# Kernel optimization log

Hardware: AMD Instinct MI355X
Metric: run time of the kernel (lower is better)

Reference implementation:

```python
import jax, jax.numpy as jnp
import numpy as np

B, L, E = 256, 500, 300  # bsz, max_doc_len, word_embed_dim
KS = [3, 5, 7]           # filters_size


def setup_inputs() -> dict:
    key = jax.random.key(0)
    ks = jax.random.split(key, 1 + 2 * len(KS))
    inp = {"x": jax.random.normal(ks[0], (B, L, E), jnp.float32)}
    i = 1
    for k in KS:
        # PyTorch Conv2d default init scale ~ 1/sqrt(fan_in)
        inp[f"aw{k}"] = jax.random.normal(ks[i], (k, E), jnp.float32) / np.sqrt(k * E).astype(np.float32); i += 1
        inp[f"ab{k}"] = jnp.zeros((1,), jnp.float32)
        inp[f"cw{k}"] = jax.random.normal(ks[i], (E,), jnp.float32) / np.sqrt(E).astype(np.float32); i += 1
        inp[f"cb{k}"] = jnpp = jnp.zeros((1,), jnp.float32)
    return inp


def _branch(x, aw, ab, cw, cb):
    # x: (B, L, E); aw: (k, E); cw: (E,)
    k = aw.shape[0]
    p = (k - 1) // 2
    x4 = x[:, None, :, :]            # NCHW: (B, 1, L, E)
    w4 = aw[None, None, :, :]        # OIHW: (1, 1, k, E)
    s = jax.lax.conv_general_dilated(x4, w4, window_strides=(1, 1),
                                     padding=((p, p), (0, 0)))  # (B, 1, L, 1)
    score = jax.nn.sigmoid(s + ab[0])[:, 0, :, :]               # (B, L, 1)
    gated = x * score                                           # broadcast over E
    # Conv2d(1,1,(1,E)) == per-timestep dot product over E
    return jnp.tanh(jnp.einsum('ble,e->bl', gated, cw) + cb[0])  # (B, L)


def reference(x, aw3, ab3, cw3, cb3, aw5, ab5, cw5, cb5, aw7, ab7, cw7, cb7):
    return (_branch(x, aw3, ab3, cw3, cb3),
            _branch(x, aw5, ab5, cw5, cb5),
            _branch(x, aw7, ab7, cw7, cb7))
```

## Files before the change

### kernel.cpp

```cpp
#include <hip/hip_runtime.h>
#include <math.h>

#define BB 256
#define LL 500
#define EE 300
#define NROWS (BB * LL)
#define ND 18
#define WSTR 20
#define KT 16
#define NTILES 19
#define KPAD (NTILES * KT)
#define WR 64
#define OPW 58
#define JPB 9
#define XSTR 17
#define DSTR 19


__global__ void wt_transpose(
    const float* __restrict__ aw3, const float* __restrict__ aw5,
    const float* __restrict__ aw7, const float* __restrict__ cw3,
    const float* __restrict__ cw5, const float* __restrict__ cw7,
    float* __restrict__ wt)
{
    const int idx = blockIdx.x * 256 + threadIdx.x;
    if (idx >= KPAD * WSTR) return;
    const int k = idx / WSTR;
    const int d = idx - k * WSTR;
    float v = 0.0f;
    if (k < EE && d < ND) {
        if      (d < 3)  v = aw3[d * EE + k];
        else if (d == 3) v = cw3[k];
        else if (d < 9)  v = aw5[(d - 4) * EE + k];
        else if (d == 9) v = cw5[k];
        else if (d < 17) v = aw7[(d - 10) * EE + k];
        else             v = cw7[k];
    }
    wt[idx] = v;
}

__global__ __launch_bounds__(256) void fused_kernel(
    const float* __restrict__ x, const float* __restrict__ wt,
    const float* __restrict__ ab3, const float* __restrict__ cb3,
    const float* __restrict__ ab5, const float* __restrict__ cb5,
    const float* __restrict__ ab7, const float* __restrict__ cb7,
    float* __restrict__ out)
{
    __shared__ float xlds[4][2][WR * XSTR];

    const int tid   = threadIdx.x;
    const int wave  = tid >> 6;
    const int lane  = tid & 63;
    const int job   = blockIdx.x * 4 + wave;
    const int batch = job / JPB;
    const int t     = job - batch * JPB;
    const int l0    = t * OPW - 3;

    const float* xbb = x + (size_t)batch * LL * EE;
    float* xw = &xlds[wave][0][0];

    const int srow = lane >> 2;
    const int sc   = lane & 3;

    const float* srp[4];
#pragma unroll
    for (int p = 0; p < 4; ++p) {
        int l = l0 + srow + p * 16;
        l = l < 0 ? 0 : (l >= LL ? LL - 1 : l);
        srp[p] = xbb + (size_t)l * EE;
    }

    float4 g[4];
#pragma unroll
    for (int p = 0; p < 4; ++p) g[p] = *(const float4*)(srp[p] + sc * 4);
#pragma unroll
    for (int p = 0; p < 4; ++p) {
        const int base = (srow + p * 16) * XSTR + sc * 4;
        xw[base + 0] = g[p].x; xw[base + 1] = g[p].y;
        xw[base + 2] = g[p].z; xw[base + 3] = g[p].w;
    }

    float acc[ND];
#pragma unroll
    for (int d = 0; d < ND; ++d) acc[d] = 0.0f;

#pragma unroll 1
    for (int tt = 0; tt < NTILES; ++tt) {
        const int nt = tt + 1;
        if (nt < NTILES) {
            const int k0 = nt * KT;
            const bool tail = (nt == NTILES - 1) && (sc == 3);
#pragma unroll
            for (int p = 0; p < 4; ++p) {
                if (tail) { g[p].x = 0.f; g[p].y = 0.f; g[p].z = 0.f; g[p].w = 0.f; }
                else      { g[p] = *(const float4*)(srp[p] + k0 + sc * 4); }
            }
        }

        const float* xb   = xw + (tt & 1) * (WR * XSTR) + lane * XSTR;
        const float* wrow = wt + tt * KT * WSTR;

        float xv[KT];
#pragma unroll
        for (int kk = 0; kk < KT; ++kk) xv[kk] = xb[kk];
#pragma unroll
        for (int kk = 0; kk < KT; ++kk) {
#pragma unroll
            for (int d = 0; d < ND; ++d)
                acc[d] = fmaf(wrow[kk * WSTR + d], xv[kk], acc[d]);
        }

        if (nt < NTILES) {
            float* xn = xw + (nt & 1) * (WR * XSTR);
#pragma unroll
            for (int p = 0; p < 4; ++p) {
                const int base = (srow + p * 16) * XSTR + sc * 4;
                xn[base + 0] = g[p].x; xn[base + 1] = g[p].y;
                xn[base + 2] = g[p].z; xn[base + 3] = g[p].w;
            }
        }
    }

    {
        const int lg = l0 + lane;
        const float vf = (lg >= 0 && lg < LL) ? 1.0f : 0.0f;
#pragma unroll
        for (int d = 0; d < ND; ++d) xw[lane * DSTR + d] = acc[d] * vf;
    }
    asm volatile("s_waitcnt lgkmcnt(0)" ::: "memory");

    if (lane >= 3 && lane < 3 + OPW) {
        const int lo = l0 + lane;
        if (lo < LL) {
            const int r = batch * LL + lo;
            const float cen3 = xw[lane * DSTR + 3];
            const float cen5 = xw[lane * DSTR + 9];
            const float cen7 = xw[lane * DSTR + 17];
            {
                float pre = 0.0f;
#pragma unroll
                for (int tp = 0; tp < 3; ++tp) pre += xw[(lane + tp - 1) * DSTR + tp];
                const float s = 1.0f / (1.0f + expf(-(pre + ab3[0])));
                out[r] = tanhf(s * cen3 + cb3[0]);
            }
            {
                float pre = 0.0f;
#pragma unroll
                for (int tp = 0; tp < 5; ++tp) pre += xw[(lane + tp - 2) * DSTR + 4 + tp];
                const float s = 1.0f / (1.0f + expf(-(pre + ab5[0])));
                out[NROWS + r] = tanhf(s * cen5 + cb5[0]);
            }
            {
                float pre = 0.0f;
#pragma unroll
                for (int tp = 0; tp < 7; ++tp) pre += xw[(lane + tp - 3) * DSTR + 10 + tp];
                const float s = 1.0f / (1.0f + expf(-(pre + ab7[0])));
                out[2 * NROWS + r] = tanhf(s * cen7 + cb7[0]);
            }
        }
    }
}

extern "C" void kernel_launch(void* const* d_in, const int* in_sizes, int n_in,
                              void* d_out, int out_size, void* d_ws, size_t ws_size,
                              hipStream_t stream) {
    const float* x   = (const float*)d_in[0];
    const float* aw3 = (const float*)d_in[1];
    const float* ab3 = (const float*)d_in[2];
    const float* cw3 = (const float*)d_in[3];
    const float* cb3 = (const float*)d_in[4];
    const float* aw5 = (const float*)d_in[5];
    const float* ab5 = (const float*)d_in[6];
    const float* cw5 = (const float*)d_in[7];
    const float* cb5 = (const float*)d_in[8];
    const float* aw7 = (const float*)d_in[9];
    const float* ab7 = (const float*)d_in[10];
    const float* cw7 = (const float*)d_in[11];
    const float* cb7 = (const float*)d_in[12];

    float* wt  = (float*)d_ws;
    float* out = (float*)d_out;

    wt_transpose<<<(KPAD * WSTR + 255) / 256, 256, 0, stream>>>(
        aw3, aw5, aw7, cw3, cw5, cw7, wt);

    fused_kernel<<<(BB * JPB) / 4, 256, 0, stream>>>(
        x, wt, ab3, cb3, ab5, cb5, ab7, cb7, out);
}
```

Before: 292.2 us.

## Split output channels across waves sharing one block-wide LDS x tile

```diff
diff --git a/kernel.cpp b/kernel.cpp
--- a/kernel.cpp
+++ b/kernel.cpp
@@ -5,16 +5,16 @@
 #define LL 500
 #define EE 300
 #define NROWS (BB * LL)
-#define ND 18
-#define WSTR 20
-#define KT 16
-#define NTILES 19
-#define KPAD (NTILES * KT)
+#define NDP 20
+#define NDW 5
+#define KT 32
+#define NT 10
+#define KPAD (NT * KT)
 #define WR 64
 #define OPW 58
 #define JPB 9
-#define XSTR 17
-#define DSTR 19
+#define XSTR 33
+#define DSTR 21
 
 
 __global__ void wt_transpose(
@@ -24,11 +24,11 @@
     float* __restrict__ wt)
 {
     const int idx = blockIdx.x * 256 + threadIdx.x;
-    if (idx >= KPAD * WSTR) return;
-    const int k = idx / WSTR;
-    const int d = idx - k * WSTR;
+    if (idx >= NDP * KPAD) return;
+    const int d = idx / KPAD;
+    const int k = idx - d * KPAD;
     float v = 0.0f;
-    if (k < EE && d < ND) {
+    if (k < EE && d < 18) {
         if      (d < 3)  v = aw3[d * EE + k];
         else if (d == 3) v = cw3[k];
         else if (d < 9)  v = aw5[(d - 4) * EE + k];
@@ -46,114 +46,105 @@
     const float* __restrict__ ab7, const float* __restrict__ cb7,
     float* __restrict__ out)
 {
-    __shared__ float xlds[4][2][WR * XSTR];
+    __shared__ float xlds[2][WR * XSTR];
+    __shared__ float dlds[WR * DSTR];
 
     const int tid   = threadIdx.x;
     const int wave  = tid >> 6;
     const int lane  = tid & 63;
-    const int job   = blockIdx.x * 4 + wave;
-    const int batch = job / JPB;
-    const int t     = job - batch * JPB;
+    const int batch = blockIdx.x / JPB;
+    const int t     = blockIdx.x - batch * JPB;
     const int l0    = t * OPW - 3;
 
     const float* xbb = x + (size_t)batch * LL * EE;
-    float* xw = &xlds[wave][0][0];
 
-    const int srow = lane >> 2;
-    const int sc   = lane & 3;
-
-    const float* srp[4];
-#pragma unroll
-    for (int p = 0; p < 4; ++p) {
-        int l = l0 + srow + p * 16;
-        l = l < 0 ? 0 : (l >= LL ? LL - 1 : l);
-        srp[p] = xbb + (size_t)l * EE;
+    const int srow = tid >> 2;
+    const int sc0  = (tid & 3) * 2;
+    const float4* srp;
+    {
+        int gl = l0 + srow;
+        gl = gl < 0 ? 0 : (gl >= LL ? LL - 1 : gl);
+        srp = (const float4*)(xbb + (size_t)gl * EE);
     }
 
-    float4 g[4];
-#pragma unroll
-    for (int p = 0; p < 4; ++p) g[p] = *(const float4*)(srp[p] + sc * 4);
-#pragma unroll
-    for (int p = 0; p < 4; ++p) {
-        const int base = (srow + p * 16) * XSTR + sc * 4;
-        xw[base + 0] = g[p].x; xw[base + 1] = g[p].y;
-        xw[base + 2] = g[p].z; xw[base + 3] = g[p].w;
+    float4 g0, g1;
+#define STAGE_LOAD(k0)                                                      \
+    {                                                                       \
+        const int f0 = (k0) / 4 + sc0;                                      \
+        g0 = (f0 < 75)     ? srp[f0]     : float4{0.f, 0.f, 0.f, 0.f};      \
+        g1 = (f0 + 1 < 75) ? srp[f0 + 1] : float4{0.f, 0.f, 0.f, 0.f};      \
+    }
+#define STAGE_WRITE(buf)                                                    \
+    {                                                                       \
+        float* dst = &xlds[buf][srow * XSTR + sc0 * 4];                     \
+        dst[0] = g0.x; dst[1] = g0.y; dst[2] = g0.z; dst[3] = g0.w;         \
+        dst[4] = g1.x; dst[5] = g1.y; dst[6] = g1.z; dst[7] = g1.w;         \
     }
 
-    float acc[ND];
+    STAGE_LOAD(0)
+    STAGE_WRITE(0)
+    __syncthreads();
+
+    const float* wd = wt + (size_t)(wave * NDW) * KPAD;
+
+    float acc[NDW];
 #pragma unroll
-    for (int d = 0; d < ND; ++d) acc[d] = 0.0f;
+    for (int d = 0; d < NDW; ++d) acc[d] = 0.0f;
 
 #pragma unroll 1
-    for (int tt = 0; tt < NTILES; ++tt) {
-        const int nt = tt + 1;
-        if (nt < NTILES) {
-            const int k0 = nt * KT;
-            const bool tail = (nt == NTILES - 1) && (sc == 3);
+    for (int tt = 0; tt < NT; ++tt) {
+        if (tt + 1 < NT) { STAGE_LOAD((tt + 1) * KT) }
+
+        const float* xb = &xlds[tt & 1][lane * XSTR];
+        const float* wk = wd + tt * KT;
 #pragma unroll
-            for (int p = 0; p < 4; ++p) {
-                if (tail) { g[p].x = 0.f; g[p].y = 0.f; g[p].z = 0.f; g[p].w = 0.f; }
-                else      { g[p] = *(const float4*)(srp[p] + k0 + sc * 4); }
-            }
+        for (int kc = 0; kc < KT; ++kc) {
+            const float xv = xb[kc];
+#pragma unroll
+            for (int d = 0; d < NDW; ++d)
+                acc[d] = fmaf(wk[d * KPAD + kc], xv, acc[d]);
         }
 
-        const float* xb   = xw + (tt & 1) * (WR * XSTR) + lane * XSTR;
-        const float* wrow = wt + tt * KT * WSTR;
-
-        float xv[KT];
-#pragma unroll
-        for (int kk = 0; kk < KT; ++kk) xv[kk] = xb[kk];
-#pragma unroll
-        for (int kk = 0; kk < KT; ++kk) {
-#pragma unroll
-            for (int d = 0; d < ND; ++d)
-                acc[d] = fmaf(wrow[kk * WSTR + d], xv[kk], acc[d]);
-        }
-
-        if (nt < NTILES) {
-            float* xn = xw + (nt & 1) * (WR * XSTR);
-#pragma unroll
-            for (int p = 0; p < 4; ++p) {
-                const int base = (srow + p * 16) * XSTR + sc * 4;
-                xn[base + 0] = g[p].x; xn[base + 1] = g[p].y;
-                xn[base + 2] = g[p].z; xn[base + 3] = g[p].w;
-            }
-        }
+        if (tt + 1 < NT) { STAGE_WRITE((tt + 1) & 1) }
+        __syncthreads();
     }
+#undef STAGE_LOAD
+#undef STAGE_WRITE
 
     {
-        const int lg = l0 + lane;
-        const float vf = (lg >= 0 && lg < LL) ? 1.0f : 0.0f;
+        const int gr = l0 + lane;
+        const float vf = (gr >= 0 && gr < LL) ? 1.0f : 0.0f;
 #pragma unroll
-        for (int d = 0; d < ND; ++d) xw[lane * DSTR + d] = acc[d] * vf;
+        for (int d = 0; d < NDW; ++d)
+            dlds[lane * DSTR + wave * NDW + d] = acc[d] * vf;
     }
-    asm volatile("s_waitcnt lgkmcnt(0)" ::: "memory");
+    __syncthreads();
 
-    if (lane >= 3 && lane < 3 + OPW) {
+    if (wave == 0 && lane >= 3 && lane < 3 + OPW) {
         const int lo = l0 + lane;
         if (lo < LL) {
             const int r = batch * LL + lo;
-            const float cen3 = xw[lane * DSTR + 3];
-            const float cen5 = xw[lane * DSTR + 9];
-            const float cen7 = xw[lane * DSTR + 17];
+            const float cen3 = dlds[lane * DSTR + 3];
+            const float cen5 = dlds[lane * DSTR + 9];
+            const float cen7 = dlds[lane * DSTR + 17];
             {
                 float pre = 0.0f;
 #pragma unroll
-                for (int tp = 0; tp < 3; ++tp) pre += xw[(lane + tp - 1) * DSTR + tp];
+                for (int tp = 0; tp < 3; ++tp) pre += dlds[(lane + tp - 1) * DSTR + tp];
                 const float s = 1.0f / (1.0f + expf(-(pre + ab3[0])));
                 out[r] = tanhf(s * cen3 + cb3[0]);
             }
             {
                 float pre = 0.0f;
 #pragma unroll
-                for (int tp = 0; tp < 5; ++tp) pre += xw[(lane + tp - 2) * DSTR + 4 + tp];
+                for (int tp = 0; tp < 5; ++tp) pre += dlds[(lane + tp - 2) * DSTR + 4 + tp];
                 const float s = 1.0f / (1.0f + expf(-(pre + ab5[0])));
                 out[NROWS + r] = tanhf(s * cen5 + cb5[0]);
             }
             {
                 float pre = 0.0f;
 #pragma unroll
-                for (int tp = 0; tp < 7; ++tp) pre += xw[(lane + tp - 3) * DSTR + 10 + tp];
+                for (int tp = 0; tp < 7; ++tp) pre += dlds[(lane + tp - 3) * DSTR + 10 + tp];
                 const float s = 1.0f / (1.0f + expf(-(pre + ab7[0])));
                 out[2 * NROWS + r] = tanhf(s * cen7 + cb7[0]);
             }
@@ -181,9 +172,9 @@
     float* wt  = (float*)d_ws;
     float* out = (float*)d_out;
 
-    wt_transpose<<<(KPAD * WSTR + 255) / 256, 256, 0, stream>>>(
+    wt_transpose<<<(NDP * KPAD + 255) / 256, 256, 0, stream>>>(
         aw3, aw5, aw7, cw3, cw5, cw7, wt);
 
-    fused_kernel<<<(BB * JPB) / 4, 256, 0, stream>>>(
+    fused_kernel<<<BB * JPB, 256, 0, stream>>>(
         x, wt, ab3, cb3, ab5, cb5, ab7, cb7, out);
 }
```

Measured after the change: 346.5 us. 18.6% more time.

## Replace scalar FMA projection with split-bf16 MFMA 32x32x16 matrix instructions

Applied to the files above, without the earlier changes.

```diff
diff --git a/kernel.cpp b/kernel.cpp
--- a/kernel.cpp
+++ b/kernel.cpp
@@ -6,47 +6,66 @@
 #define EE 300
 #define NROWS (BB * LL)
 #define ND 18
-#define WSTR 20
-#define KT 16
-#define NTILES 19
-#define KPAD (NTILES * KT)
-#define WR 64
-#define OPW 58
-#define JPB 9
-#define XSTR 17
+#define KSTEPS 19
+#define OPJ 26
+#define JPB 20
 #define DSTR 19
 
 
-__global__ void wt_transpose(
+typedef short bf16x8 __attribute__((ext_vector_type(8)));
+typedef float f32x16 __attribute__((ext_vector_type(16)));
+
+__global__ void wfrag_build(
     const float* __restrict__ aw3, const float* __restrict__ aw5,
     const float* __restrict__ aw7, const float* __restrict__ cw3,
     const float* __restrict__ cw5, const float* __restrict__ cw7,
-    float* __restrict__ wt)
+    unsigned int* __restrict__ wf)
 {
     const int idx = blockIdx.x * 256 + threadIdx.x;
-    if (idx >= KPAD * WSTR) return;
-    const int k = idx / WSTR;
-    const int d = idx - k * WSTR;
-    float v = 0.0f;
-    if (k < EE && d < ND) {
-        if      (d < 3)  v = aw3[d * EE + k];
-        else if (d == 3) v = cw3[k];
-        else if (d < 9)  v = aw5[(d - 4) * EE + k];
-        else if (d == 9) v = cw5[k];
-        else if (d < 17) v = aw7[(d - 10) * EE + k];
-        else             v = cw7[k];
+    const int s    = idx >> 9;
+    const int r9   = idx & 511;
+    const int lane = r9 >> 3;
+    const int q    = r9 & 7;
+    const int half = lane >> 5;
+    const int d    = lane & 31;
+    const bool hiPart = (q < 4);
+    const int qq   = q & 3;
+
+    unsigned int outw = 0;
+#pragma unroll
+    for (int e = 0; e < 2; ++e) {
+        const int k = s * 16 + half * 8 + qq * 2 + e;
+        float w = 0.0f;
+        if (d < ND && k < EE) {
+            if      (d < 3)  w = aw3[d * EE + k];
+            else if (d == 3) w = cw3[k];
+            else if (d < 9)  w = aw5[(d - 4) * EE + k];
+            else if (d == 9) w = cw5[k];
+            else if (d < 17) w = aw7[(d - 10) * EE + k];
+            else             w = cw7[k];
+        }
+        const unsigned int u = __float_as_uint(w);
+        unsigned short h;
+        if (hiPart) {
+            h = (unsigned short)(u >> 16);
+        } else {
+            const float whi = __uint_as_float(u & 0xFFFF0000u);
+            const float lo  = w - whi;
+            h = (unsigned short)(__float_as_uint(lo) >> 16);
+        }
+        outw |= ((unsigned int)h) << (16 * e);
     }
-    wt[idx] = v;
+    wf[idx] = outw;
 }
 
 __global__ __launch_bounds__(256) void fused_kernel(
-    const float* __restrict__ x, const float* __restrict__ wt,
+    const float* __restrict__ x, const unsigned int* __restrict__ wf,
     const float* __restrict__ ab3, const float* __restrict__ cb3,
     const float* __restrict__ ab5, const float* __restrict__ cb5,
     const float* __restrict__ ab7, const float* __restrict__ cb7,
     float* __restrict__ out)
 {
-    __shared__ float xlds[4][2][WR * XSTR];
+    __shared__ float dlds[4][32 * DSTR];
 
     const int tid   = threadIdx.x;
     const int wave  = tid >> 6;
@@ -54,108 +73,97 @@
     const int job   = blockIdx.x * 4 + wave;
     const int batch = job / JPB;
     const int t     = job - batch * JPB;
-    const int l0    = t * OPW - 3;
+    const int l0    = t * OPJ - 3;
 
-    const float* xbb = x + (size_t)batch * LL * EE;
-    float* xw = &xlds[wave][0][0];
+    const int row  = lane & 31;
+    const int half = lane >> 5;
+    int gr = l0 + row;
+    gr = gr < 0 ? 0 : (gr >= LL ? LL - 1 : gr);
+    const float* xr = x + ((size_t)batch * LL + gr) * EE + half * 8;
 
-    const int srow = lane >> 2;
-    const int sc   = lane & 3;
+    const uint4* wfv = (const uint4*)wf;
 
-    const float* srp[4];
+    float4 xa = *(const float4*)(xr + 0);
+    float4 xb = *(const float4*)(xr + 4);
+    uint4  bh = wfv[(0 * 64 + lane) * 2 + 0];
+    uint4  bl = wfv[(0 * 64 + lane) * 2 + 1];
+
+    f32x16 acc;
 #pragma unroll
-    for (int p = 0; p < 4; ++p) {
-        int l = l0 + srow + p * 16;
-        l = l < 0 ? 0 : (l >= LL ? LL - 1 : l);
-        srp[p] = xbb + (size_t)l * EE;
+    for (int i = 0; i < 16; ++i) acc[i] = 0.0f;
+
+#pragma unroll 1
+    for (int s = 0; s < KSTEPS; ++s) {
+        float4 xa_n, xb_n; uint4 bh_n, bl_n;
+        if (s + 1 < KSTEPS) {
+            const int ko = (s + 1) * 16;
+            xa_n = *(const float4*)(xr + ko);
+            const int off2 = ((s + 1 == KSTEPS - 1) && half) ? 0 : 4;
+            xb_n = *(const float4*)(xr + ko + off2);
+            bh_n = wfv[((s + 1) * 64 + lane) * 2 + 0];
+            bl_n = wfv[((s + 1) * 64 + lane) * 2 + 1];
+        }
+
+        bf16x8 ahi, alo;
+        const float xf[8] = {xa.x, xa.y, xa.z, xa.w, xb.x, xb.y, xb.z, xb.w};
+#pragma unroll
+        for (int e = 0; e < 8; ++e) {
+            const unsigned int u = __float_as_uint(xf[e]);
+            ahi[e] = (short)(u >> 16);
+            const float hif = __uint_as_float(u & 0xFFFF0000u);
+            const float lo  = xf[e] - hif;
+            alo[e] = (short)(__float_as_uint(lo) >> 16);
+        }
+        const bf16x8 bhi = __builtin_bit_cast(bf16x8, bh);
+        const bf16x8 blo = __builtin_bit_cast(bf16x8, bl);
+
+        acc = __builtin_amdgcn_mfma_f32_32x32x16_bf16(ahi, bhi, acc, 0, 0, 0);
+        acc = __builtin_amdgcn_mfma_f32_32x32x16_bf16(ahi, blo, acc, 0, 0, 0);
+        acc = __builtin_amdgcn_mfma_f32_32x32x16_bf16(alo, bhi, acc, 0, 0, 0);
+
+        if (s + 1 < KSTEPS) { xa = xa_n; xb = xb_n; bh = bh_n; bl = bl_n; }
     }
 
-    float4 g[4];
+    float* dl = dlds[wave];
+    const int d = lane & 31;
+    if (d < ND) {
 #pragma unroll
-    for (int p = 0; p < 4; ++p) g[p] = *(const float4*)(srp[p] + sc * 4);
-#pragma unroll
-    for (int p = 0; p < 4; ++p) {
-        const int base = (srow + p * 16) * XSTR + sc * 4;
-        xw[base + 0] = g[p].x; xw[base + 1] = g[p].y;
-        xw[base + 2] = g[p].z; xw[base + 3] = g[p].w;
-    }
-
-    float acc[ND];
-#pragma unroll
-    for (int d = 0; d < ND; ++d) acc[d] = 0.0f;
-
-#pragma unroll 1
-    for (int tt = 0; tt < NTILES; ++tt) {
-        const int nt = tt + 1;
-        if (nt < NTILES) {
-            const int k0 = nt * KT;
-            const bool tail = (nt == NTILES - 1) && (sc == 3);
-#pragma unroll
-            for (int p = 0; p < 4; ++p) {
-                if (tail) { g[p].x = 0.f; g[p].y = 0.f; g[p].z = 0.f; g[p].w = 0.f; }
-                else      { g[p] = *(const float4*)(srp[p] + k0 + sc * 4); }
-            }
+        for (int i = 0; i < 16; ++i) {
+            const int rw = (i & 3) + 8 * (i >> 2) + 4 * half;
+            const int g  = l0 + rw;
+            const float vf = (g >= 0 && g < LL) ? 1.0f : 0.0f;
+            dl[rw * DSTR + d] = acc[i] * vf;
         }
-
-        const float* xb   = xw + (tt & 1) * (WR * XSTR) + lane * XSTR;
-        const float* wrow = wt + tt * KT * WSTR;
-
-        float xv[KT];
-#pragma unroll
-        for (int kk = 0; kk < KT; ++kk) xv[kk] = xb[kk];
-#pragma unroll
-        for (int kk = 0; kk < KT; ++kk) {
-#pragma unroll
-            for (int d = 0; d < ND; ++d)
-                acc[d] = fmaf(wrow[kk * WSTR + d], xv[kk], acc[d]);
-        }
-
-        if (nt < NTILES) {
-            float* xn = xw + (nt & 1) * (WR * XSTR);
-#pragma unroll
-            for (int p = 0; p < 4; ++p) {
-                const int base = (srow + p * 16) * XSTR + sc * 4;
-                xn[base + 0] = g[p].x; xn[base + 1] = g[p].y;
-                xn[base + 2] = g[p].z; xn[base + 3] = g[p].w;
-            }
-        }
-    }
-
-    {
-        const int lg = l0 + lane;
-        const float vf = (lg >= 0 && lg < LL) ? 1.0f : 0.0f;
-#pragma unroll
-        for (int d = 0; d < ND; ++d) xw[lane * DSTR + d] = acc[d] * vf;
     }
     asm volatile("s_waitcnt lgkmcnt(0)" ::: "memory");
 
-    if (lane >= 3 && lane < 3 + OPW) {
-        const int lo = l0 + lane;
-        if (lo < LL) {
-            const int r = batch * LL + lo;
-            const float cen3 = xw[lane * DSTR + 3];
-            const float cen5 = xw[lane * DSTR + 9];
-            const float cen7 = xw[lane * DSTR + 17];
+    if (lane >= 3 && lane < 3 + OPJ) {
+        const int lo_ = l0 + lane;
+        if (lo_ < LL) {
+            const int r = batch * LL + lo_;
+            const float cen3 = dl[lane * DSTR + 3];
+            const float cen5 = dl[lane * DSTR + 9];
+            const float cen7 = dl[lane * DSTR + 17];
             {
                 float pre = 0.0f;
 #pragma unroll
-                for (int tp = 0; tp < 3; ++tp) pre += xw[(lane + tp - 1) * DSTR + tp];
-                const float s = 1.0f / (1.0f + expf(-(pre + ab3[0])));
-                out[r] = tanhf(s * cen3 + cb3[0]);
+                for (int tp = 0; tp < 3; ++tp) pre += dl[(lane + tp - 1) * DSTR + tp];
+                const float sg = 1.0f / (1.0f + expf(-(pre + ab3[0])));
+                out[r] = tanhf(sg * cen3 + cb3[0]);
             }
             {
                 float pre = 0.0f;
 #pragma unroll
-                for (int tp = 0; tp < 5; ++tp) pre += xw[(lane + tp - 2) * DSTR + 4 + tp];
-                const float s = 1.0f / (1.0f + expf(-(pre + ab5[0])));
-                out[NROWS + r] = tanhf(s * cen5 + cb5[0]);
+                for (int tp = 0; tp < 5; ++tp) pre += dl[(lane + tp - 2) * DSTR + 4 + tp];
+                const float sg = 1.0f / (1.0f + expf(-(pre + ab5[0])));
+                out[NROWS + r] = tanhf(sg * cen5 + cb5[0]);
             }
             {
                 float pre = 0.0f;
 #pragma unroll
-                for (int tp = 0; tp < 7; ++tp) pre += xw[(lane + tp - 3) * DSTR + 10 + tp];
-                const float s = 1.0f / (1.0f + expf(-(pre + ab7[0])));
-                out[2 * NROWS + r] = tanhf(s * cen7 + cb7[0]);
+                for (int tp = 0; tp < 7; ++tp) pre += dl[(lane + tp - 3) * DSTR + 10 + tp];
+                const float sg = 1.0f / (1.0f + expf(-(pre + ab7[0])));
+                out[2 * NROWS + r] = tanhf(sg * cen7 + cb7[0]);
             }
         }
     }
@@ -178,12 +186,11 @@
     const float* cw7 = (const float*)d_in[11];
     const float* cb7 = (const float*)d_in[12];
 
-    float* wt  = (float*)d_ws;
+    unsigned int* wf = (unsigned int*)d_ws;
     float* out = (float*)d_out;
 
-    wt_transpose<<<(KPAD * WSTR + 255) / 256, 256, 0, stream>>>(
-        aw3, aw5, aw7, cw3, cw5, cw7, wt);
+    wfrag_build<<<38, 256, 0, stream>>>(aw3, aw5, aw7, cw3, cw5, cw7, wf);
 
     fused_kernel<<<(BB * JPB) / 4, 256, 0, stream>>>(
-        x, wt, ab3, cb3, ab5, cb5, ab7, cb7, out);
+        x, wf, ab3, cb3, ab5, cb5, ab7, cb7, out);
 }
```

New measurement: 256.5 us. 1.14x faster.
